# Kernel optimization log

Hardware: AMD Instinct MI355X
Metric: run time of the kernel (lower is better)

The kernel has to match this reference:

```python
import math
import jax, jax.numpy as jnp
import numpy as np

HIDDEN = 2048
N_HEAD = 32
N_KV = 8
HEAD_DIM = HIDDEN // N_HEAD  # 64
B, S = 2, 2048


def setup_inputs() -> dict:
    key = jax.random.key(0)
    ks = jax.random.split(key, 9)
    sc_h = 1.0 / math.sqrt(HIDDEN)
    return {
        "X": jax.random.normal(ks[0], (B, S, HIDDEN), jnp.float32),
        "Wq": jax.random.normal(ks[1], (HIDDEN, HIDDEN), jnp.float32) * sc_h,
        "bq": jax.random.normal(ks[2], (HIDDEN,), jnp.float32) * 0.01,
        "Wk": jax.random.normal(ks[3], (N_KV * HEAD_DIM, HIDDEN), jnp.float32) * sc_h,
        "bk": jax.random.normal(ks[4], (N_KV * HEAD_DIM,), jnp.float32) * 0.01,
        "Wv": jax.random.normal(ks[5], (N_KV * HEAD_DIM, HIDDEN), jnp.float32) * sc_h,
        "bv": jax.random.normal(ks[6], (N_KV * HEAD_DIM,), jnp.float32) * 0.01,
        "Wo": jax.random.normal(ks[7], (HIDDEN, HIDDEN), jnp.float32) * sc_h,
        "bo": jax.random.normal(ks[8], (HIDDEN,), jnp.float32) * 0.01,
    }


def reference(X, Wq, bq, Wk, bk, Wv, bv, Wo, bo):
    b, s, _ = X.shape
    g = N_HEAD // N_KV  # query heads per kv head (repeat_interleave group)
    scale = 1.0 / math.sqrt(HEAD_DIM)

    q = X @ Wq.T + bq                       # [B,S,H*D]
    k = X @ Wk.T + bk                       # [B,S,KV*D]
    v = X @ Wv.T + bv                       # [B,S,KV*D]

    # q grouped as (B, KV, g, S, D): head h = kv*g + j matches repeat_interleave on dim=1
    q = q.reshape(b, s, N_KV, g, HEAD_DIM).transpose(0, 2, 3, 1, 4)  # [B,KV,g,S,D]
    k = k.reshape(b, s, N_KV, HEAD_DIM).transpose(0, 2, 1, 3)         # [B,KV,S,D]
    v = v.reshape(b, s, N_KV, HEAD_DIM).transpose(0, 2, 1, 3)         # [B,KV,S,D]

    # scores without materializing repeated K/V: broadcast kv head over g query heads
    scores = jnp.einsum("bkgqd,bkld->bkgql", q, k) * scale            # [B,KV,g,S,S]
    weights = jax.nn.softmax(scores, axis=-1)
    out = jnp.einsum("bkgql,bkld->bkgqd", weights, v)                 # [B,KV,g,S,D]

    # replicate torch's contiguous .view(B, seq, -1) applied to the [B,H,S,D]
    # tensor WITHOUT transposing back: plain row-major reshape of (B,H,S,D).
    out = out.reshape(b, s, N_HEAD * HEAD_DIM)
    return out @ Wo.T + bo
```

## Files before the change

kernel.cpp:

```cpp
#include <hip/hip_runtime.h>

#define HIDDEN 2048
#define NHEADS 32
#define NKV    8
#define HDIM   64
#define BATCH  2
#define SEQ    2048
#define MROWS  (BATCH*SEQ)
#define NQKV   3072

#define SCALEQ 0.18033688011112042f

typedef _Float16 half8_t __attribute__((ext_vector_type(8)));
typedef _Float16 half4_t __attribute__((ext_vector_type(4)));
typedef __fp16   fp16x2_t __attribute__((ext_vector_type(2)));
typedef float    f32x4_t __attribute__((ext_vector_type(4)));

#define AS1 __attribute__((address_space(1)))
#define AS3 __attribute__((address_space(3)))

__device__ __forceinline__ void async_copy16(void* lds, const void* g) {
    __builtin_amdgcn_global_load_lds((AS1 void*)g, (AS3 void*)lds, 16, 0, 0);
}

template <typename OutT, bool QKV>
__global__ __launch_bounds__(256) void gemm_nt(
    const _Float16* __restrict__ A, const _Float16* __restrict__ Bm,
    const float* __restrict__ bias, OutT* __restrict__ C,
    _Float16* __restrict__ kfb, _Float16* __restrict__ vfb,
    int M, int N, int K, int ldc) {
    __shared__ _Float16 As[128 * 32];
    __shared__ _Float16 Bs[128 * 32];

    const int tid  = threadIdx.x;
    const int wave = tid >> 6;
    const int lane = tid & 63;
    const int quad = lane >> 4;
    const int l16  = lane & 15;
    const int m0 = blockIdx.y * 128;
    const int n0 = blockIdx.x * 128;
    const int mw = (wave & 1) * 64;
    const int nw = (wave >> 1) * 64;

    f32x4_t acc[4][4] = {};

    const int srow = tid >> 2;
    const int scol = (tid & 3) * 8;
    const _Float16* Ag = A  + (size_t)(m0 + srow) * K + scol;
    const _Float16* Bg = Bm + (size_t)(n0 + srow) * K + scol;
    char* AsB = (char*)As + (size_t)wave * 1024;
    char* BsB = (char*)Bs + (size_t)wave * 1024;

    for (int k0 = 0; k0 < K; k0 += 32) {
        __syncthreads();
        async_copy16(AsB,        Ag + k0);
        async_copy16(AsB + 4096, Ag + (size_t)64 * K + k0);
        async_copy16(BsB,        Bg + k0);
        async_copy16(BsB + 4096, Bg + (size_t)64 * K + k0);
        __syncthreads();

        half8_t a[4], b[4];
#pragma unroll
        for (int i = 0; i < 4; ++i)
            a[i] = *(const half8_t*)(As + (mw + i * 16 + l16) * 32 + quad * 8);
#pragma unroll
        for (int i = 0; i < 4; ++i)
            b[i] = *(const half8_t*)(Bs + (nw + i * 16 + l16) * 32 + quad * 8);
#pragma unroll
        for (int mi = 0; mi < 4; ++mi)
#pragma unroll
            for (int ni = 0; ni < 4; ++ni)
                acc[mi][ni] = __builtin_amdgcn_mfma_f32_16x16x32_f16(
                    a[mi], b[ni], acc[mi][ni], 0, 0, 0);
    }

    if (QKV && n0 >= 2560) {
#pragma unroll
        for (int mi = 0; mi < 4; ++mi) {
#pragma unroll
            for (int ni = 0; ni < 4; ++ni) {
                const int c  = n0 + nw + ni * 16 + l16;
                const int kd = c - 2560;
                const int kv = kd >> 6, d = kd & 63;
                const float bv = bias[c];
                const int r0 = m0 + mw + mi * 16 + quad * 4;
                const int bb = r0 >> 11;
                const int sblk = (r0 & 2047) >> 6;
                const int nt = (r0 >> 4) & 3;
                const int dt = (d >> 4) & 3;
                half4_t h;
#pragma unroll
                for (int i = 0; i < 4; ++i) h[i] = (_Float16)(acc[mi][ni][i] + bv);
                *(half4_t*)(vfb + ((size_t)(bb * 8 + kv) * 32 + sblk) * 4096 +
                            ((nt * 4 + dt) * 64 + quad * 16 + (d & 15)) * 4) = h;
            }
        }
    } else if (QKV && n0 >= 2048) {
#pragma unroll
        for (int mi = 0; mi < 4; ++mi) {
#pragma unroll
            for (int ni = 0; ni < 4; ++ni) {
                const int c  = n0 + nw + ni * 16 + l16;
                const int kd = c - 2048;
                const int kv = kd >> 6, d = kd & 63;
                const float bv = bias[c];
                const int r0 = m0 + mw + mi * 16 + quad * 4;
                const int bb = r0 >> 11;
                const int sblk = (r0 & 2047) >> 6;
                const int nt = (r0 >> 4) & 3;
                _Float16* dst = kfb + ((size_t)(bb * 8 + kv) * 32 + sblk) * 4096 +
                    ((nt * 2 + (d >> 5)) * 64 + ((d >> 3) & 3) * 16 + quad * 4) * 8 +
                    (d & 7);
#pragma unroll
                for (int i = 0; i < 4; ++i)
                    dst[i * 8] = (_Float16)(acc[mi][ni][i] + bv);
            }
        }
    } else {
#pragma unroll
        for (int mi = 0; mi < 4; ++mi) {
#pragma unroll
            for (int ni = 0; ni < 4; ++ni) {
                const int c = n0 + nw + ni * 16 + l16;
                const float bv = bias[c];
#pragma unroll
                for (int i = 0; i < 4; ++i) {
                    const int r = m0 + mw + mi * 16 + quad * 4 + i;
                    C[(size_t)r * ldc + c] = (OutT)(acc[mi][ni][i] + bv);
                }
            }
        }
    }
}

__global__ __launch_bounds__(256, 2) void attn_kernel(
    const _Float16* __restrict__ Qb, const _Float16* __restrict__ Kf,
    const _Float16* __restrict__ Vf, _Float16* __restrict__ ctx) {
    __shared__ _Float16 Ks[2][4096];
    __shared__ _Float16 Vs[2][4096];

    const int tid  = threadIdx.x;
    const int wave = tid >> 6;
    const int lane = tid & 63;
    const int quad = lane >> 4;
    const int l16  = lane & 15;
    const int qt  = blockIdx.x;
    const int bkv = blockIdx.y;
    const int b   = bkv >> 3;
    const int kv  = bkv & 7;
    const int h   = kv * 4 + wave;

    half8_t qa[4][2];
#pragma unroll
    for (int g = 0; g < 4; ++g) {
        const _Float16* qp = Qb + ((size_t)(b * SEQ + qt * 64 + g * 16 + l16)) * HIDDEN
                              + h * 64 + quad * 8;
        qa[g][0] = *(const half8_t*)qp;
        qa[g][1] = *(const half8_t*)(qp + 32);
    }

    f32x4_t ot[4][4] = {};
    f32x4_t lacc[4] = {};
    const half4_t ones = {(_Float16)1.f, (_Float16)1.f, (_Float16)1.f, (_Float16)1.f};

    const size_t kvbase = (size_t)(b * 8 + kv) * 32 * 4096;
    const int sh = (wave * 2) * 512 + lane * 8;

#pragma unroll
    for (int j = 0; j < 2; ++j) {
        async_copy16(&Ks[0][(wave * 2 + j) * 512], Kf + kvbase + sh + j * 512);
        async_copy16(&Vs[0][(wave * 2 + j) * 512], Vf + kvbase + sh + j * 512);
    }

    for (int kt = 0; kt < SEQ / 64; ++kt) {
        __syncthreads();
        const int cur = kt & 1;
        if (kt + 1 < SEQ / 64) {
            const int nxt = cur ^ 1;
            const size_t off = kvbase + (size_t)(kt + 1) * 4096 + sh;
#pragma unroll
            for (int j = 0; j < 2; ++j) {
                async_copy16(&Ks[nxt][(wave * 2 + j) * 512], Kf + off + j * 512);
                async_copy16(&Vs[nxt][(wave * 2 + j) * 512], Vf + off + j * 512);
            }
        }

        half8_t kf[4][2];
#pragma unroll
        for (int nt = 0; nt < 4; ++nt) {
#pragma unroll
            for (int c = 0; c < 2; ++c)
                kf[nt][c] = *(const half8_t*)(&Ks[cur][((nt * 2 + c) * 64 + lane) * 8]);
        }

        half4_t p[4][4];
#pragma unroll
        for (int g = 0; g < 4; ++g) {
#pragma unroll
            for (int nt = 0; nt < 4; ++nt) {
                f32x4_t s = {};
                s = __builtin_amdgcn_mfma_f32_16x16x32_f16(kf[nt][0], qa[g][0], s, 0, 0, 0);
                s = __builtin_amdgcn_mfma_f32_16x16x32_f16(kf[nt][1], qa[g][1], s, 0, 0, 0);
                const fp16x2_t lo = __builtin_amdgcn_cvt_pkrtz(
                    __builtin_amdgcn_exp2f(s[0]), __builtin_amdgcn_exp2f(s[1]));
                const fp16x2_t hi = __builtin_amdgcn_cvt_pkrtz(
                    __builtin_amdgcn_exp2f(s[2]), __builtin_amdgcn_exp2f(s[3]));
                half4_t pv;
                pv[0] = (_Float16)lo[0]; pv[1] = (_Float16)lo[1];
                pv[2] = (_Float16)hi[0]; pv[3] = (_Float16)hi[1];
                p[g][nt] = pv;
                lacc[g] = __builtin_amdgcn_mfma_f32_16x16x16f16(ones, pv, lacc[g], 0, 0, 0);
            }
        }

#pragma unroll
        for (int nt = 0; nt < 4; ++nt) {
#pragma unroll
            for (int dt = 0; dt < 4; ++dt) {
                const half4_t vf = *(const half4_t*)(&Vs[cur][((nt * 4 + dt) * 64 + lane) * 4]);
#pragma unroll
                for (int g = 0; g < 4; ++g)
                    ot[g][dt] = __builtin_amdgcn_mfma_f32_16x16x16f16(
                        vf, p[g][nt], ot[g][dt], 0, 0, 0);
            }
        }
    }

    __syncthreads();
    _Float16* T = &Ks[0][0] + wave * 1152;
#pragma unroll
    for (int g = 0; g < 4; ++g) {
        const float inv = 1.f / lacc[g][0];
#pragma unroll
        for (int dt = 0; dt < 4; ++dt) {
            half4_t hh;
#pragma unroll
            for (int r = 0; r < 4; ++r) hh[r] = (_Float16)(ot[g][dt][r] * inv);
            *(half4_t*)(T + l16 * 72 + dt * 16 + quad * 4) = hh;
        }
        __builtin_amdgcn_s_waitcnt(0);
        _Float16* cp = ctx + (((size_t)b * 32 + h) * SEQ + qt * 64 + g * 16 + l16) * 64;
#pragma unroll
        for (int pass = 0; pass < 2; ++pass) {
            const half8_t row = *(const half8_t*)(T + l16 * 72 + pass * 32 + quad * 8);
            *(half8_t*)(cp + pass * 32 + quad * 8) = row;
        }
        __builtin_amdgcn_s_waitcnt(0);
    }
}

__device__ __forceinline__ void cast4(const float* __restrict__ s,
                                      _Float16* __restrict__ d, int i, float sc) {
    const f32x4_t v = ((const f32x4_t*)s)[i];
    half4_t h;
#pragma unroll
    for (int j = 0; j < 4; ++j) h[j] = (_Float16)(v[j] * sc);
    ((half4_t*)d)[i] = h;
}

__global__ __launch_bounds__(256) void prep(
    const float* __restrict__ X,  const float* __restrict__ Wq,
    const float* __restrict__ Wk, const float* __restrict__ Wv,
    const float* __restrict__ Wo, const float* __restrict__ bq,
    const float* __restrict__ bk, const float* __restrict__ bv,
    _Float16* __restrict__ Xh, _Float16* __restrict__ Wqkv,
    _Float16* __restrict__ Woh, float* __restrict__ bqkv) {
    const int bid = blockIdx.x, tid = threadIdx.x;
    if (bid < 8192)       cast4(X,  Xh,   bid * 256 + tid, 1.f);
    else if (bid < 12288) cast4(Wq, Wqkv, (bid - 8192) * 256 + tid, SCALEQ);
    else if (bid < 13312) cast4(Wk, Wqkv + (size_t)HIDDEN * HIDDEN, (bid - 12288) * 256 + tid, 1.f);
    else if (bid < 14336) cast4(Wv, Wqkv + (size_t)(HIDDEN + 512) * HIDDEN, (bid - 13312) * 256 + tid, 1.f);
    else if (bid < 18432) cast4(Wo, Woh,  (bid - 14336) * 256 + tid, 1.f);
    else {
        const int i = (bid - 18432) * 256 + tid;
        if (i < 2048)      bqkv[i] = bq[i] * SCALEQ;
        else if (i < 2560) bqkv[i] = bk[i - 2048];
        else if (i < 3072) bqkv[i] = bv[i - 2560];
    }
}

extern "C" void kernel_launch(void* const* d_in, const int* in_sizes, int n_in,
                              void* d_out, int out_size, void* d_ws, size_t ws_size,
                              hipStream_t stream) {
    const float* X  = (const float*)d_in[0];
    const float* Wq = (const float*)d_in[1];
    const float* bq = (const float*)d_in[2];
    const float* Wk = (const float*)d_in[3];
    const float* bk = (const float*)d_in[4];
    const float* Wv = (const float*)d_in[5];
    const float* bv = (const float*)d_in[6];
    const float* Wo = (const float*)d_in[7];
    const float* bo = (const float*)d_in[8];
    float* out = (float*)d_out;

    char* p = (char*)d_ws;
    _Float16* Xh   = (_Float16*)p; p += (size_t)MROWS * HIDDEN * 2;
    _Float16* Wqkv = (_Float16*)p; p += (size_t)NQKV * HIDDEN * 2;
    _Float16* Woh  = (_Float16*)p; p += (size_t)HIDDEN * HIDDEN * 2;
    float*    bqkv = (float*)p;    p += (size_t)NQKV * 4;
    _Float16* Qb   = (_Float16*)p; p += (size_t)MROWS * HIDDEN * 2;
    _Float16* Kfb  = (_Float16*)p; p += (size_t)16 * 32 * 4096 * 2;
    _Float16* Vfb  = (_Float16*)p; p += (size_t)16 * 32 * 4096 * 2;
    _Float16* ctx  = Xh;

    prep<<<18444, 256, 0, stream>>>(X, Wq, Wk, Wv, Wo, bq, bk, bv,
                                    Xh, Wqkv, Woh, bqkv);

    gemm_nt<_Float16, true><<<dim3(NQKV / 128, MROWS / 128), 256, 0, stream>>>(
        Xh, Wqkv, bqkv, Qb, Kfb, Vfb, MROWS, NQKV, HIDDEN, HIDDEN);

    attn_kernel<<<dim3(SEQ / 64, BATCH * NKV), 256, 0, stream>>>(Qb, Kfb, Vfb, ctx);

    gemm_nt<float, false><<<dim3(HIDDEN / 128, MROWS / 128), 256, 0, stream>>>(
        ctx, Woh, bo, out, nullptr, nullptr, MROWS, HIDDEN, HIDDEN, HIDDEN);
}
```

Measured before the change: 349.9 us.

## Double-buffer A tile in LDS, load B directly to registers, swizzle LDS

Restructures the GEMM main loop so the A tile is double-buffered in LDS with async global-to-LDS copies for the next k-step issued before computing the current one. The B operand now skips LDS and is prefetched straight into registers one step ahead. The LDS layout gains an XOR swizzle to cut bank conflicts. This removes one of the two barriers per iteration and overlaps loads with MFMA work, at the cost of more registers and uncoalesced per-lane B global loads. It also appears to rely on there being only one barrier between the async write into a buffer and the reads from it.

```diff
diff --git a/kernel.cpp b/kernel.cpp
--- a/kernel.cpp
+++ b/kernel.cpp
@@ -29,8 +29,7 @@
     const float* __restrict__ bias, OutT* __restrict__ C,
     _Float16* __restrict__ kfb, _Float16* __restrict__ vfb,
     int M, int N, int K, int ldc) {
-    __shared__ _Float16 As[128 * 32];
-    __shared__ _Float16 Bs[128 * 32];
+    __shared__ _Float16 As[2][128 * 32];
 
     const int tid  = threadIdx.x;
     const int wave = tid >> 6;
@@ -45,34 +44,51 @@
     f32x4_t acc[4][4] = {};
 
     const int srow = tid >> 2;
-    const int scol = (tid & 3) * 8;
-    const _Float16* Ag = A  + (size_t)(m0 + srow) * K + scol;
-    const _Float16* Bg = Bm + (size_t)(n0 + srow) * K + scol;
-    char* AsB = (char*)As + (size_t)wave * 1024;
-    char* BsB = (char*)Bs + (size_t)wave * 1024;
-
-    for (int k0 = 0; k0 < K; k0 += 32) {
-        __syncthreads();
-        async_copy16(AsB,        Ag + k0);
-        async_copy16(AsB + 4096, Ag + (size_t)64 * K + k0);
-        async_copy16(BsB,        Bg + k0);
-        async_copy16(BsB + 4096, Bg + (size_t)64 * K + k0);
-        __syncthreads();
-
-        half8_t a[4], b[4];
-#pragma unroll
-        for (int i = 0; i < 4; ++i)
-            a[i] = *(const half8_t*)(As + (mw + i * 16 + l16) * 32 + quad * 8);
-#pragma unroll
-        for (int i = 0; i < 4; ++i)
-            b[i] = *(const half8_t*)(Bs + (nw + i * 16 + l16) * 32 + quad * 8);
-#pragma unroll
-        for (int mi = 0; mi < 4; ++mi)
-#pragma unroll
-            for (int ni = 0; ni < 4; ++ni)
-                acc[mi][ni] = __builtin_amdgcn_mfma_f32_16x16x32_f16(
-                    a[mi], b[ni], acc[mi][ni], 0, 0, 0);
-    }
+    const int sgr  = (tid & 3) ^ (srow & 3);
+    const _Float16* Ag = A + (size_t)(m0 + srow) * K + sgr * 8;
+    const int woffA = wave * 512;
+
+    const _Float16* Bg = Bm + (size_t)(n0 + nw + l16) * K + quad * 8;
+
+    const int iters = K >> 5;
+    const int rsw = quad ^ (l16 & 3);
+
+    half8_t b0[4], b1[4];
+
+    async_copy16(&As[0][woffA],        Ag);
+    async_copy16(&As[0][woffA + 2048], Ag + (size_t)64 * K);
+#pragma unroll
+    for (int i = 0; i < 4; ++i)
+        b0[i] = *(const half8_t*)(Bg + (size_t)i * 16 * K);
+
+#define GEMM_STEP(BUF, BCUR, BNXT, KNEXT)                                     \
+    {                                                                         \
+        __syncthreads();                                                      \
+        if ((KNEXT) < K) {                                                    \
+            async_copy16(&As[(BUF) ^ 1][woffA],        Ag + (KNEXT));         \
+            async_copy16(&As[(BUF) ^ 1][woffA + 2048],                        \
+                         Ag + (size_t)64 * K + (KNEXT));                      \
+            _Pragma("unroll")                                                 \
+            for (int i = 0; i < 4; ++i)                                       \
+                BNXT[i] = *(const half8_t*)(Bg + (size_t)i * 16 * K + (KNEXT)); \
+        }                                                                     \
+        half8_t a[4];                                                         \
+        _Pragma("unroll")                                                     \
+        for (int i = 0; i < 4; ++i)                                           \
+            a[i] = *(const half8_t*)(&As[BUF][(mw + i * 16 + l16) * 32 + rsw * 8]); \
+        _Pragma("unroll")                                                     \
+        for (int mi = 0; mi < 4; ++mi)                                        \
+            _Pragma("unroll")                                                 \
+            for (int ni = 0; ni < 4; ++ni)                                    \
+                acc[mi][ni] = __builtin_amdgcn_mfma_f32_16x16x32_f16(         \
+                    a[mi], BCUR[ni], acc[mi][ni], 0, 0, 0);                   \
+    }
+
+    for (int it = 0; it < iters; it += 2) {
+        GEMM_STEP(0, b0, b1, (it + 1) << 5)
+        GEMM_STEP(1, b1, b0, (it + 2) << 5)
+    }
+#undef GEMM_STEP
 
     if (QKV && n0 >= 2560) {
 #pragma unroll
```

Result: slower. 404.8 us (+15.7%).
